# Kernel optimization log

Measured on AMD Instinct MI355X. Metric: run time of the kernel, lower is better.

## Reference

```python
import jax, jax.numpy as jnp
import numpy as np

N = 100000   # nodes
E = 600000   # edges
DIN = 128
H = 128
DOUT = 64
EPS = 1e-5   # BatchNorm1d default eps


def setup_inputs() -> dict:
    key = jax.random.key(0)
    ks = jax.random.split(key, 16)
    w = lambda k, shape: jax.random.normal(k, shape, jnp.float32) * 0.05
    return {
        "x": jax.random.normal(ks[0], (N, DIN), jnp.float32),
        "edge_index": jax.random.randint(ks[1], (2, E), 0, N),
        # layer 1: SAGEConv(DIN -> H)  (lin_l on aggregated neighbors w/ bias, lin_r on root)
        "Wl1": w(ks[2], (DIN, H)), "bl1": jnp.zeros((H,), jnp.float32), "Wr1": w(ks[3], (DIN, H)),
        "g1": jnp.ones((H,), jnp.float32), "be1": jnp.zeros((H,), jnp.float32),
        "rm1": jax.random.normal(ks[4], (H,), jnp.float32) * 0.1,
        "rv1": jax.random.uniform(ks[5], (H,), jnp.float32, 0.5, 1.5),
        # layer 2: SAGEConv(H -> H)
        "Wl2": w(ks[6], (H, H)), "bl2": jnp.zeros((H,), jnp.float32), "Wr2": w(ks[7], (H, H)),
        "g2": jnp.ones((H,), jnp.float32), "be2": jnp.zeros((H,), jnp.float32),
        "rm2": jax.random.normal(ks[8], (H,), jnp.float32) * 0.1,
        "rv2": jax.random.uniform(ks[9], (H,), jnp.float32, 0.5, 1.5),
        # layer 3: SAGEConv(H -> DOUT), no BN/ReLU after
        "Wl3": w(ks[10], (H, DOUT)), "bl3": jnp.zeros((DOUT,), jnp.float32), "Wr3": w(ks[11], (H, DOUT)),
    }


def _sage_conv(x, src, dst, Wl, bl, Wr):
    # mean-aggregate source features at targets, then lin_l(agg) + b + lin_r(x)
    agg = jax.ops.segment_sum(x[src], dst, num_segments=N)          # [N, d]
    deg = jax.ops.segment_sum(jnp.ones((src.shape[0],), x.dtype), dst, num_segments=N)
    agg = agg / jnp.maximum(deg, 1.0)[:, None]
    return agg @ Wl + bl + x @ Wr


def _bn_eval(h, g, b, rm, rv):
    return (h - rm) * (g * jax.lax.rsqrt(rv + EPS)) + b


def reference(x, edge_index, Wl1, bl1, Wr1, g1, be1, rm1, rv1,
              Wl2, bl2, Wr2, g2, be2, rm2, rv2, Wl3, bl3, Wr3):
    src, dst = edge_index[0], edge_index[1]
    h = jax.nn.relu(_bn_eval(_sage_conv(x, src, dst, Wl1, bl1, Wr1), g1, be1, rm1, rv1))
    h = jax.nn.relu(_bn_eval(_sage_conv(h, src, dst, Wl2, bl2, Wr2), g2, be2, rm2, rv2))
    return _sage_conv(h, src, dst, Wl3, bl3, Wr3)   # [N, DOUT]
```

## Files before the change

### kernel.cpp

```cpp
#include <hip/hip_runtime.h>

#define CAP 48

typedef short  s8v  __attribute__((ext_vector_type(8)));
typedef float  f4v  __attribute__((ext_vector_type(4)));

__device__ __forceinline__ unsigned short f2bf(float f) {
    unsigned u = __float_as_uint(f);
    u += 0x7FFFu + ((u >> 16) & 1u);
    return (unsigned short)(u >> 16);
}
__device__ __forceinline__ float bflo(unsigned v) { return __uint_as_float(v << 16); }
__device__ __forceinline__ float bfhi(unsigned v) { return __uint_as_float(v & 0xffff0000u); }

#define ACC8(A_, v) do { (A_)[0]+=bflo((v).x); (A_)[1]+=bfhi((v).x); (A_)[2]+=bflo((v).y); (A_)[3]+=bfhi((v).y); \
                         (A_)[4]+=bflo((v).z); (A_)[5]+=bfhi((v).z); (A_)[6]+=bflo((v).w); (A_)[7]+=bfhi((v).w); } while(0)

__global__ __launch_bounds__(256) void k_prep(const int* __restrict__ src, const int* __restrict__ dst, int E,
                                              int* __restrict__ cnt, int* __restrict__ bucket,
                                              const float* __restrict__ x, unsigned short* __restrict__ xb, int n4,
                                              const float* W0, const float* W1, const float* W2,
                                              const float* W3, const float* W4, const float* W5,
                                              unsigned short* P0, unsigned short* P1, unsigned short* P2,
                                              unsigned short* P3, unsigned short* P4, unsigned short* P5,
                                              const float* g1, const float* be1, const float* rm1, const float* rv1, const float* bl1,
                                              const float* g2, const float* be2, const float* rm2, const float* rv2, const float* bl2,
                                              float* P,
                                              unsigned short* hb, unsigned short* hb2, unsigned short* t3b, int N,
                                              int nbBucket, int nbCvt) {
    int b = blockIdx.x;
    const int tid = threadIdx.x;
    if (b < nbBucket) {
        int e = b * 256 + tid;
        if (e < E) {
            int d = dst[e];
            int slot = atomicAdd(&cnt[d], 1);
            if (slot < CAP) bucket[(size_t)d * CAP + slot] = src[e];
        }
        return;
    }
    b -= nbBucket;
    if (b < nbCvt) {
        int i = b * 256 + tid;
        if (i < n4) {
            float4 v = ((const float4*)x)[i];
            ushort4 o;
            o.x = f2bf(v.x); o.y = f2bf(v.y); o.z = f2bf(v.z); o.w = f2bf(v.w);
            ((ushort4*)xb)[i] = o;
        }
        return;
    }
    b -= nbCvt;
    const int px = b & 63;
    const int py = b >> 6;
    if (py == 6) {
        if (px == 0 && tid < 128) {
            int i = tid;
            float s1 = g1[i] * rsqrtf(rv1[i] + 1e-5f);
            P[i]       = s1;
            P[128 + i] = (bl1[i] - rm1[i]) * s1 + be1[i];
            float s2 = g2[i] * rsqrtf(rv2[i] + 1e-5f);
            P[256 + i] = s2;
            P[384 + i] = (bl2[i] - rm2[i]) * s2 + be2[i];
            xb [(size_t)N * 128 + i] = 0;
            hb [(size_t)N * 128 + i] = 0;
            hb2[(size_t)N * 128 + i] = 0;
            if (i < 64) t3b[(size_t)N * 64 + i] = 0;
        }
        return;
    }
    const float* W; unsigned short* Pk; int JD;
    switch (py) {
        case 0: W = W0; Pk = P0; JD = 128; break;
        case 1: W = W1; Pk = P1; JD = 128; break;
        case 2: W = W2; Pk = P2; JD = 128; break;
        case 3: W = W3; Pk = P3; JD = 128; break;
        case 4: W = W4; Pk = P4; JD = 64;  break;
        default:W = W5; Pk = P5; JD = 64;  break;
    }
    int o = px * 256 + tid;
    if (o >= 128 * JD) return;
    int j    = o & 7;
    int lane = (o >> 3) & 63;
    int t    = o >> 9;
    int nt   = t % (JD / 16);
    int kt   = t / (JD / 16);
    int k = kt * 32 + (lane >> 4) * 8 + j;
    int nn = nt * 16 + (lane & 15);
    Pk[o] = f2bf(W[(size_t)k * JD + nn]);
}

template<bool T3>
__global__ __launch_bounds__(256) void k_fused(const unsigned short* __restrict__ feat,
                                               const int* __restrict__ cnt, const int* __restrict__ bucket,
                                               const unsigned short* __restrict__ Bl, const unsigned short* __restrict__ Br,
                                               const float* __restrict__ scale, const float* __restrict__ shift,
                                               unsigned short* __restrict__ out,
                                               const unsigned short* __restrict__ W3p, unsigned short* __restrict__ t3,
                                               int n, int units) {
    __shared__ unsigned short sA[32 * 136];
    __shared__ unsigned short sH[T3 ? 32 * 136 : 8];
    const int tid  = threadIdx.x;
    const int wave = tid >> 6;
    const int lane = tid & 63;

    for (int u = blockIdx.x; u < units; u += gridDim.x) {
        const int nb0 = u * 32;

        {
            const int q4   = lane >> 4;
            const int li   = lane & 15;
            const int base = q4 << 4;
            const uint4* inp = (const uint4*)feat;
            int rows[2], cs[2], idxs[2];
            #pragma unroll
            for (int t = 0; t < 2; t++) {
                rows[t] = wave * 8 + t * 4 + q4;
                int node = nb0 + rows[t];
                bool ok = node < n;
                int c = ok ? cnt[node] : 0; if (c > CAP) c = CAP;
                cs[t] = c;
                idxs[t] = (ok && li < c) ? bucket[(size_t)node * CAP + li] : n;
            }
            #pragma unroll
            for (int t = 0; t < 2; t++) {
                const int c = cs[t];
                float a[8] = {0.f, 0.f, 0.f, 0.f, 0.f, 0.f, 0.f, 0.f};
                if (c > 0) {
                    #pragma unroll
                    for (int uu = 0; uu < 8; uu++) {
                        int idx = __shfl(idxs[t], base + uu);
                        uint4 v = inp[(size_t)idx * 16 + li];
                        ACC8(a, v);
                    }
                }
                if (c > 8) {
                    #pragma unroll
                    for (int uu = 8; uu < 16; uu++) {
                        int idx = __shfl(idxs[t], base + uu);
                        uint4 v = inp[(size_t)idx * 16 + li];
                        ACC8(a, v);
                    }
                }
                const int node = nb0 + rows[t];
                for (int s = 16; s < c; s++) {
                    int idx = bucket[(size_t)node * CAP + s];
                    uint4 v = inp[(size_t)idx * 16 + li];
                    ACC8(a, v);
                }
                if (node < n) {
                    float iv = 1.0f / fmaxf((float)c, 1.0f);
                    uint4 o;
                    o.x = (unsigned)f2bf(a[0] * iv) | ((unsigned)f2bf(a[1] * iv) << 16);
                    o.y = (unsigned)f2bf(a[2] * iv) | ((unsigned)f2bf(a[3] * iv) << 16);
                    o.z = (unsigned)f2bf(a[4] * iv) | ((unsigned)f2bf(a[5] * iv) << 16);
                    o.w = (unsigned)f2bf(a[6] * iv) | ((unsigned)f2bf(a[7] * iv) << 16);
                    *(uint4*)(sA + rows[t] * 136 + li * 8) = o;
                }
            }
        }
        __syncthreads();

        const int m = lane & 15;
        const int q = lane >> 4;
        const int nt0 = wave * 2;
        const int rg0 = min(nb0 + m,      n - 1);
        const int rg1 = min(nb0 + 16 + m, n - 1);

        f4v acc[2][2];
        #pragma unroll
        for (int mt = 0; mt < 2; mt++)
            #pragma unroll
            for (int c = 0; c < 2; c++) {
                acc[mt][c][0] = 0.f; acc[mt][c][1] = 0.f; acc[mt][c][2] = 0.f; acc[mt][c][3] = 0.f;
            }

        #pragma unroll
        for (int kt = 0; kt < 4; kt++) {
            const int ko = kt * 32 + q * 8;
            s8v a0 = *(const s8v*)(sA + m * 136 + ko);
            s8v a1 = *(const s8v*)(sA + (16 + m) * 136 + ko);
            s8v a0d = *(const s8v*)(feat + (size_t)rg0 * 128 + ko);
            s8v a1d = *(const s8v*)(feat + (size_t)rg1 * 128 + ko);
            #pragma unroll
            for (int c = 0; c < 2; c++) {
                s8v b  = *(const s8v*)(Bl + ((size_t)(kt * 8 + nt0 + c) * 64 + lane) * 8);
                acc[0][c] = __builtin_amdgcn_mfma_f32_16x16x32_bf16(a0, b, acc[0][c], 0, 0, 0);
                acc[1][c] = __builtin_amdgcn_mfma_f32_16x16x32_bf16(a1, b, acc[1][c], 0, 0, 0);
                s8v b2 = *(const s8v*)(Br + ((size_t)(kt * 8 + nt0 + c) * 64 + lane) * 8);
                acc[0][c] = __builtin_amdgcn_mfma_f32_16x16x32_bf16(a0d, b2, acc[0][c], 0, 0, 0);
                acc[1][c] = __builtin_amdgcn_mfma_f32_16x16x32_bf16(a1d, b2, acc[1][c], 0, 0, 0);
            }
        }

        float scv[2], shv[2];
        #pragma unroll
        for (int c = 0; c < 2; c++) {
            int col = (nt0 + c) * 16 + m;
            scv[c] = scale[col]; shv[c] = shift[col];
        }
        #pragma unroll
        for (int mt = 0; mt < 2; mt++) {
            #pragma unroll
            for (int reg = 0; reg < 4; reg++) {
                int rloc = mt * 16 + q * 4 + reg;
                int row  = nb0 + rloc;
                if (row < n) {
                    #pragma unroll
                    for (int c = 0; c < 2; c++) {
                        int col = (nt0 + c) * 16 + m;
                        float v = fmaxf(acc[mt][c][reg] * scv[c] + shv[c], 0.f);
                        unsigned short uq = f2bf(v);
                        out[(size_t)row * 128 + col] = uq;
                        if constexpr (T3) sH[rloc * 136 + col] = uq;
                    }
                }
            }
        }

        if constexpr (T3) {
            __syncthreads();
            f4v a3c[2];
            #pragma unroll
            for (int mt = 0; mt < 2; mt++) { a3c[mt][0] = 0.f; a3c[mt][1] = 0.f; a3c[mt][2] = 0.f; a3c[mt][3] = 0.f; }
            #pragma unroll
            for (int kt = 0; kt < 4; kt++) {
                const int ko = kt * 32 + q * 8;
                s8v a0 = *(const s8v*)(sH + m * 136 + ko);
                s8v a1 = *(const s8v*)(sH + (16 + m) * 136 + ko);
                s8v b  = *(const s8v*)(W3p + ((size_t)(kt * 4 + wave) * 64 + lane) * 8);
                a3c[0] = __builtin_amdgcn_mfma_f32_16x16x32_bf16(a0, b, a3c[0], 0, 0, 0);
                a3c[1] = __builtin_amdgcn_mfma_f32_16x16x32_bf16(a1, b, a3c[1], 0, 0, 0);
            }
            #pragma unroll
            for (int mt = 0; mt < 2; mt++) {
                #pragma unroll
                for (int reg = 0; reg < 4; reg++) {
                    int row = nb0 + mt * 16 + q * 4 + reg;
                    if (row < n) t3[(size_t)row * 64 + wave * 16 + m] = f2bf(a3c[mt][reg]);
                }
            }
        }
        __syncthreads();
    }
}

__global__ __launch_bounds__(256) void k_final(const unsigned short* __restrict__ hb2,
                                               const unsigned short* __restrict__ t3,
                                               const int* __restrict__ cnt, const int* __restrict__ bucket,
                                               const unsigned short* __restrict__ Bp, const float* __restrict__ bias,
                                               float* __restrict__ outf, int n, int units) {
    __shared__ float sG[32 * 68];
    const int tid  = threadIdx.x;
    const int wave = tid >> 6;
    const int lane = tid & 63;

    for (int u = blockIdx.x; u < units; u += gridDim.x) {
        const int nb0 = u * 32;

        {
            const int e8   = lane >> 3;
            const int li   = lane & 7;
            const int base = e8 << 3;
            const uint4* inp = (const uint4*)t3;
            const int row  = wave * 8 + e8;
            const int node = nb0 + row;
            const bool ok  = node < n;
            int c = ok ? cnt[node] : 0; if (c > CAP) c = CAP;
            int idx1 = (ok && li < c)     ? bucket[(size_t)node * CAP + li]     : n;
            int idx2 = (ok && li + 8 < c) ? bucket[(size_t)node * CAP + li + 8] : n;
            float a[8] = {0.f, 0.f, 0.f, 0.f, 0.f, 0.f, 0.f, 0.f};
            if (c > 0) {
                #pragma unroll
                for (int uu = 0; uu < 8; uu++) {
                    int idx = __shfl(idx1, base + uu);
                    uint4 v = inp[(size_t)idx * 8 + li];
                    ACC8(a, v);
                }
            }
            if (c > 8) {
                #pragma unroll
                for (int uu = 0; uu < 8; uu++) {
                    int idx = __shfl(idx2, base + uu);
                    uint4 v = inp[(size_t)idx * 8 + li];
                    ACC8(a, v);
                }
            }
            for (int s = 16; s < c; s++) {
                int idx = bucket[(size_t)node * CAP + s];
                uint4 v = inp[(size_t)idx * 8 + li];
                ACC8(a, v);
            }
            if (ok) {
                float iv = 1.0f / fmaxf((float)c, 1.0f);
                float4 o1; o1.x = a[0] * iv; o1.y = a[1] * iv; o1.z = a[2] * iv; o1.w = a[3] * iv;
                float4 o2; o2.x = a[4] * iv; o2.y = a[5] * iv; o2.z = a[6] * iv; o2.w = a[7] * iv;
                *(float4*)(sG + row * 68 + li * 8)     = o1;
                *(float4*)(sG + row * 68 + li * 8 + 4) = o2;
            }
        }
        __syncthreads();

        const int m = lane & 15;
        const int q = lane >> 4;
        const int rg0 = min(nb0 + m,      n - 1);
        const int rg1 = min(nb0 + 16 + m, n - 1);

        f4v acc[2];
        #pragma unroll
        for (int mt = 0; mt < 2; mt++) { acc[mt][0] = 0.f; acc[mt][1] = 0.f; acc[mt][2] = 0.f; acc[mt][3] = 0.f; }

        #pragma unroll
        for (int kt = 0; kt < 4; kt++) {
            const int ko = kt * 32 + q * 8;
            s8v a0 = *(const s8v*)(hb2 + (size_t)rg0 * 128 + ko);
            s8v a1 = *(const s8v*)(hb2 + (size_t)rg1 * 128 + ko);
            s8v b  = *(const s8v*)(Bp + ((size_t)(kt * 4 + wave) * 64 + lane) * 8);
            acc[0] = __builtin_amdgcn_mfma_f32_16x16x32_bf16(a0, b, acc[0], 0, 0, 0);
            acc[1] = __builtin_amdgcn_mfma_f32_16x16x32_bf16(a1, b, acc[1], 0, 0, 0);
        }

        const int col = wave * 16 + m;
        const float bv = bias[col];
        #pragma unroll
        for (int mt = 0; mt < 2; mt++) {
            #pragma unroll
            for (int reg = 0; reg < 4; reg++) {
                int rloc = mt * 16 + q * 4 + reg;
                int row  = nb0 + rloc;
                if (row < n) outf[(size_t)row * 64 + col] = acc[mt][reg] + sG[rloc * 68 + col] + bv;
            }
        }
        __syncthreads();
    }
}

extern "C" void kernel_launch(void* const* d_in, const int* in_sizes, int n_in,
                              void* d_out, int out_size, void* d_ws, size_t ws_size,
                              hipStream_t stream) {
    const float* x   = (const float*)d_in[0];
    const int*   ei  = (const int*)d_in[1];
    const float* Wl1 = (const float*)d_in[2];
    const float* bl1 = (const float*)d_in[3];
    const float* Wr1 = (const float*)d_in[4];
    const float* g1  = (const float*)d_in[5];
    const float* be1 = (const float*)d_in[6];
    const float* rm1 = (const float*)d_in[7];
    const float* rv1 = (const float*)d_in[8];
    const float* Wl2 = (const float*)d_in[9];
    const float* bl2 = (const float*)d_in[10];
    const float* Wr2 = (const float*)d_in[11];
    const float* g2  = (const float*)d_in[12];
    const float* be2 = (const float*)d_in[13];
    const float* rm2 = (const float*)d_in[14];
    const float* rv2 = (const float*)d_in[15];
    const float* Wl3 = (const float*)d_in[16];
    const float* bl3 = (const float*)d_in[17];
    const float* Wr3 = (const float*)d_in[18];

    const int N = in_sizes[0] / 128;
    const int E = in_sizes[1] / 2;
    const int* src = ei;
    const int* dst = ei + E;

    char* w = (char*)d_ws;
    auto au = [](size_t v) { return (v + 1023) & ~(size_t)1023; };
    size_t off = 0;
    int*            cnt    = (int*)(w + off);            off += au((size_t)N * 4);
    int*            bucket = (int*)(w + off);            off += au((size_t)N * CAP * 4);
    unsigned short* xb     = (unsigned short*)(w + off); off += au((size_t)(N + 1) * 128 * 2);
    unsigned short* hb     = (unsigned short*)(w + off); off += au((size_t)(N + 1) * 128 * 2);
    unsigned short* hb2    = (unsigned short*)(w + off); off += au((size_t)(N + 1) * 128 * 2);
    unsigned short* t3b    = (unsigned short*)(w + off); off += au((size_t)(N + 1) * 64 * 2);
    unsigned short* Wp[6];
    Wp[0] = (unsigned short*)(w + off); off += au(128 * 128 * 2);
    Wp[1] = (unsigned short*)(w + off); off += au(128 * 128 * 2);
    Wp[2] = (unsigned short*)(w + off); off += au(128 * 128 * 2);
    Wp[3] = (unsigned short*)(w + off); off += au(128 * 128 * 2);
    Wp[4] = (unsigned short*)(w + off); off += au(128 * 64 * 2);
    Wp[5] = (unsigned short*)(w + off); off += au(128 * 64 * 2);
    float* P = (float*)(w + off); off += 2048;
    (void)ws_size; (void)n_in;

    hipMemsetAsync(cnt, 0, (size_t)N * 4, stream);

    const int n4 = N * 32;
    const int nbBucket = (E + 255) / 256;
    const int nbCvt    = (n4 + 255) / 256;
    k_prep<<<nbBucket + nbCvt + 448, 256, 0, stream>>>(src, dst, E, cnt, bucket,
                                                       x, xb, n4,
                                                       Wl1, Wr1, Wl2, Wr2, Wl3, Wr3,
                                                       Wp[0], Wp[1], Wp[2], Wp[3], Wp[4], Wp[5],
                                                       g1, be1, rm1, rv1, bl1, g2, be2, rm2, rv2, bl2, P,
                                                       hb, hb2, t3b, N, nbBucket, nbCvt);

    const int units = (N + 31) / 32;
    const int grid  = (units + 1) / 2;

    k_fused<false><<<grid, 256, 0, stream>>>(xb, cnt, bucket, Wp[0], Wp[1],
                                             P, P + 128, hb, nullptr, nullptr, N, units);
    k_fused<true><<<grid, 256, 0, stream>>>(hb, cnt, bucket, Wp[2], Wp[3],
                                            P + 256, P + 384, hb2, Wp[4], t3b, N, units);
    k_final<<<grid, 256, 0, stream>>>(hb2, t3b, cnt, bucket, Wp[5], bl3, (float*)d_out, N, units);
}
```

Baseline: 305.3 us.

## Make each wave own 16 rows end to end and drop block barriers

The fused and final kernels now have each wave gather, aggregate and multiply its own 16 rows across all output columns, so no __syncthreads is needed between the gather and MFMA phases. The grid-stride loop is replaced by one 64-node block per launch index. The aim is to remove barrier stalls and let waves overlap gather latency with other waves' matrix work. In exchange each wave reloads every B tile itself, which adds L1/L2 traffic, and it holds more accumulator registers.

```diff
diff --git a/kernel.cpp b/kernel.cpp
--- a/kernel.cpp
+++ b/kernel.cpp
@@ -97,151 +97,130 @@
                                                const float* __restrict__ scale, const float* __restrict__ shift,
                                                unsigned short* __restrict__ out,
                                                const unsigned short* __restrict__ W3p, unsigned short* __restrict__ t3,
-                                               int n, int units) {
-    __shared__ unsigned short sA[32 * 136];
-    __shared__ unsigned short sH[T3 ? 32 * 136 : 8];
+                                               int n) {
+    __shared__ unsigned short sA[64 * 136];
     const int tid  = threadIdx.x;
     const int wave = tid >> 6;
     const int lane = tid & 63;
-
-    for (int u = blockIdx.x; u < units; u += gridDim.x) {
-        const int nb0 = u * 32;
-
-        {
-            const int q4   = lane >> 4;
-            const int li   = lane & 15;
-            const int base = q4 << 4;
-            const uint4* inp = (const uint4*)feat;
-            int rows[2], cs[2], idxs[2];
-            #pragma unroll
-            for (int t = 0; t < 2; t++) {
-                rows[t] = wave * 8 + t * 4 + q4;
-                int node = nb0 + rows[t];
-                bool ok = node < n;
-                int c = ok ? cnt[node] : 0; if (c > CAP) c = CAP;
-                cs[t] = c;
-                idxs[t] = (ok && li < c) ? bucket[(size_t)node * CAP + li] : n;
-            }
-            #pragma unroll
-            for (int t = 0; t < 2; t++) {
-                const int c = cs[t];
-                float a[8] = {0.f, 0.f, 0.f, 0.f, 0.f, 0.f, 0.f, 0.f};
-                if (c > 0) {
-                    #pragma unroll
-                    for (int uu = 0; uu < 8; uu++) {
-                        int idx = __shfl(idxs[t], base + uu);
-                        uint4 v = inp[(size_t)idx * 16 + li];
-                        ACC8(a, v);
-                    }
-                }
-                if (c > 8) {
-                    #pragma unroll
-                    for (int uu = 8; uu < 16; uu++) {
-                        int idx = __shfl(idxs[t], base + uu);
-                        uint4 v = inp[(size_t)idx * 16 + li];
-                        ACC8(a, v);
-                    }
-                }
-                const int node = nb0 + rows[t];
-                for (int s = 16; s < c; s++) {
-                    int idx = bucket[(size_t)node * CAP + s];
+    const int nb0  = blockIdx.x * 64;
+    const int wb   = nb0 + wave * 16;
+    if (wb >= n) return;
+
+    {
+        const int q4   = lane >> 4;
+        const int li   = lane & 15;
+        const int base = q4 << 4;
+        const uint4* inp = (const uint4*)feat;
+        int cs[4], idxs[4];
+        #pragma unroll
+        for (int t = 0; t < 4; t++) {
+            int node = wb + t * 4 + q4;
+            bool ok = node < n;
+            int c = ok ? cnt[node] : 0; if (c > CAP) c = CAP;
+            cs[t] = c;
+            idxs[t] = (ok && li < c) ? bucket[(size_t)node * CAP + li] : n;
+        }
+        #pragma unroll
+        for (int t = 0; t < 4; t++) {
+            const int c = cs[t];
+            float a[8] = {0.f, 0.f, 0.f, 0.f, 0.f, 0.f, 0.f, 0.f};
+            if (c > 0) {
+                #pragma unroll
+                for (int uu = 0; uu < 8; uu++) {
+                    int idx = __shfl(idxs[t], base + uu);
                     uint4 v = inp[(size_t)idx * 16 + li];
                     ACC8(a, v);
                 }
-                if (node < n) {
-                    float iv = 1.0f / fmaxf((float)c, 1.0f);
-                    uint4 o;
-                    o.x = (unsigned)f2bf(a[0] * iv) | ((unsigned)f2bf(a[1] * iv) << 16);
-                    o.y = (unsigned)f2bf(a[2] * iv) | ((unsigned)f2bf(a[3] * iv) << 16);
-                    o.z = (unsigned)f2bf(a[4] * iv) | ((unsigned)f2bf(a[5] * iv) << 16);
-                    o.w = (unsigned)f2bf(a[6] * iv) | ((unsigned)f2bf(a[7] * iv) << 16);
-                    *(uint4*)(sA + rows[t] * 136 + li * 8) = o;
+            }
+            if (c > 8) {
+                #pragma unroll
+                for (int uu = 8; uu < 16; uu++) {
+                    int idx = __shfl(idxs[t], base + uu);
+                    uint4 v = inp[(size_t)idx * 16 + li];
+                    ACC8(a, v);
                 }
             }
-        }
-        __syncthreads();
-
-        const int m = lane & 15;
-        const int q = lane >> 4;
-        const int nt0 = wave * 2;
-        const int rg0 = min(nb0 + m,      n - 1);
-        const int rg1 = min(nb0 + 16 + m, n - 1);
-
-        f4v acc[2][2];
-        #pragma unroll
-        for (int mt = 0; mt < 2; mt++)
-            #pragma unroll
-            for (int c = 0; c < 2; c++) {
-                acc[mt][c][0] = 0.f; acc[mt][c][1] = 0.f; acc[mt][c][2] = 0.f; acc[mt][c][3] = 0.f;
-            }
-
+            const int node = wb + t * 4 + q4;
+            for (int s = 16; s < c; s++) {
+                int idx = bucket[(size_t)node * CAP + s];
+                uint4 v = inp[(size_t)idx * 16 + li];
+                ACC8(a, v);
+            }
+            if (node < n) {
+                float iv = 1.0f / fmaxf((float)c, 1.0f);
+                uint4 o;
+                o.x = (unsigned)f2bf(a[0] * iv) | ((unsigned)f2bf(a[1] * iv) << 16);
+                o.y = (unsigned)f2bf(a[2] * iv) | ((unsigned)f2bf(a[3] * iv) << 16);
+                o.z = (unsigned)f2bf(a[4] * iv) | ((unsigned)f2bf(a[5] * iv) << 16);
+                o.w = (unsigned)f2bf(a[6] * iv) | ((unsigned)f2bf(a[7] * iv) << 16);
+                *(uint4*)(sA + (wave * 16 + t * 4 + q4) * 136 + li * 8) = o;
+            }
+        }
+    }
+
+    const int m = lane & 15;
+    const int q = lane >> 4;
+    const int arow = wave * 16 + m;
+    const int rg = min(wb + m, n - 1);
+
+    f4v acc[8];
+    #pragma unroll
+    for (int nt = 0; nt < 8; nt++) { acc[nt][0] = 0.f; acc[nt][1] = 0.f; acc[nt][2] = 0.f; acc[nt][3] = 0.f; }
+
+    #pragma unroll
+    for (int kt = 0; kt < 4; kt++) {
+        const int ko = kt * 32 + q * 8;
+        s8v a0  = *(const s8v*)(sA + arow * 136 + ko);
+        s8v a0d = *(const s8v*)(feat + (size_t)rg * 128 + ko);
+        #pragma unroll
+        for (int nt = 0; nt < 8; nt++) {
+            s8v b  = *(const s8v*)(Bl + ((size_t)(kt * 8 + nt) * 64 + lane) * 8);
+            acc[nt] = __builtin_amdgcn_mfma_f32_16x16x32_bf16(a0, b, acc[nt], 0, 0, 0);
+            s8v b2 = *(const s8v*)(Br + ((size_t)(kt * 8 + nt) * 64 + lane) * 8);
+            acc[nt] = __builtin_amdgcn_mfma_f32_16x16x32_bf16(a0d, b2, acc[nt], 0, 0, 0);
+        }
+    }
+
+    #pragma unroll
+    for (int nt = 0; nt < 8; nt++) {
+        const int col = nt * 16 + m;
+        const float sc = scale[col];
+        const float sh = shift[col];
+        #pragma unroll
+        for (int reg = 0; reg < 4; reg++) {
+            int rloc = wave * 16 + q * 4 + reg;
+            int row  = nb0 + rloc;
+            if (row < n) {
+                float v = fmaxf(acc[nt][reg] * sc + sh, 0.f);
+                unsigned short uq = f2bf(v);
+                out[(size_t)row * 128 + col] = uq;
+                if constexpr (T3) sA[rloc * 136 + col] = uq;
+            }
+        }
+    }
+
+    if constexpr (T3) {
+        f4v a3c[4];
+        #pragma unroll
+        for (int nt = 0; nt < 4; nt++) { a3c[nt][0] = 0.f; a3c[nt][1] = 0.f; a3c[nt][2] = 0.f; a3c[nt][3] = 0.f; }
         #pragma unroll
         for (int kt = 0; kt < 4; kt++) {
             const int ko = kt * 32 + q * 8;
-            s8v a0 = *(const s8v*)(sA + m * 136 + ko);
-            s8v a1 = *(const s8v*)(sA + (16 + m) * 136 + ko);
-            s8v a0d = *(const s8v*)(feat + (size_t)rg0 * 128 + ko);
-            s8v a1d = *(const s8v*)(feat + (size_t)rg1 * 128 + ko);
+            s8v a0 = *(const s8v*)(sA + arow * 136 + ko);
             #pragma unroll
-            for (int c = 0; c < 2; c++) {
-                s8v b  = *(const s8v*)(Bl + ((size_t)(kt * 8 + nt0 + c) * 64 + lane) * 8);
-                acc[0][c] = __builtin_amdgcn_mfma_f32_16x16x32_bf16(a0, b, acc[0][c], 0, 0, 0);
-                acc[1][c] = __builtin_amdgcn_mfma_f32_16x16x32_bf16(a1, b, acc[1][c], 0, 0, 0);
-                s8v b2 = *(const s8v*)(Br + ((size_t)(kt * 8 + nt0 + c) * 64 + lane) * 8);
-                acc[0][c] = __builtin_amdgcn_mfma_f32_16x16x32_bf16(a0d, b2, acc[0][c], 0, 0, 0);
-                acc[1][c] = __builtin_amdgcn_mfma_f32_16x16x32_bf16(a1d, b2, acc[1][c], 0, 0, 0);
-            }
-        }
-
-        float scv[2], shv[2];
-        #pragma unroll
-        for (int c = 0; c < 2; c++) {
-            int col = (nt0 + c) * 16 + m;
-            scv[c] = scale[col]; shv[c] = shift[col];
-        }
-        #pragma unroll
-        for (int mt = 0; mt < 2; mt++) {
+            for (int nt = 0; nt < 4; nt++) {
+                s8v b = *(const s8v*)(W3p + ((size_t)(kt * 4 + nt) * 64 + lane) * 8);
+                a3c[nt] = __builtin_amdgcn_mfma_f32_16x16x32_bf16(a0, b, a3c[nt], 0, 0, 0);
+            }
+        }
+        #pragma unroll
+        for (int nt = 0; nt < 4; nt++) {
             #pragma unroll
             for (int reg = 0; reg < 4; reg++) {
-                int rloc = mt * 16 + q * 4 + reg;
-                int row  = nb0 + rloc;
-                if (row < n) {
-                    #pragma unroll
-                    for (int c = 0; c < 2; c++) {
-                        int col = (nt0 + c) * 16 + m;
-                        float v = fmaxf(acc[mt][c][reg] * scv[c] + shv[c], 0.f);
-                        unsigned short uq = f2bf(v);
-                        out[(size_t)row * 128 + col] = uq;
-                        if constexpr (T3) sH[rloc * 136 + col] = uq;
-                    }
-                }
-            }
-        }
-
-        if constexpr (T3) {
-            __syncthreads();
-            f4v a3c[2];
-            #pragma unroll
-            for (int mt = 0; mt < 2; mt++) { a3c[mt][0] = 0.f; a3c[mt][1] = 0.f; a3c[mt][2] = 0.f; a3c[mt][3] = 0.f; }
-            #pragma unroll
-            for (int kt = 0; kt < 4; kt++) {
-                const int ko = kt * 32 + q * 8;
-                s8v a0 = *(const s8v*)(sH + m * 136 + ko);
-                s8v a1 = *(const s8v*)(sH + (16 + m) * 136 + ko);
-                s8v b  = *(const s8v*)(W3p + ((size_t)(kt * 4 + wave) * 64 + lane) * 8);
-                a3c[0] = __builtin_amdgcn_mfma_f32_16x16x32_bf16(a0, b, a3c[0], 0, 0, 0);
-                a3c[1] = __builtin_amdgcn_mfma_f32_16x16x32_bf16(a1, b, a3c[1], 0, 0, 0);
-            }
-            #pragma unroll
-            for (int mt = 0; mt < 2; mt++) {
-                #pragma unroll
-                for (int reg = 0; reg < 4; reg++) {
-                    int row = nb0 + mt * 16 + q * 4 + reg;
-                    if (row < n) t3[(size_t)row * 64 + wave * 16 + m] = f2bf(a3c[mt][reg]);
-                }
-            }
-        }
-        __syncthreads();
+                int row = nb0 + wave * 16 + q * 4 + reg;
+                if (row < n) t3[(size_t)row * 64 + nt * 16 + m] = f2bf(a3c[nt][reg]);
+            }
+        }
     }
 }
 
@@ -249,22 +228,24 @@
                                                const unsigned short* __restrict__ t3,
                                                const int* __restrict__ cnt, const int* __restrict__ bucket,
                                                const unsigned short* __restrict__ Bp, const float* __restrict__ bias,
-                                               float* __restrict__ outf, int n, int units) {
-    __shared__ float sG[32 * 68];
+                                               float* __restrict__ outf, int n) {
+    __shared__ float sG[64 * 68];
     const int tid  = threadIdx.x;
     const int wave = tid >> 6;
     const int lane = tid & 63;
-
-    for (int u = blockIdx.x; u < units; u += gridDim.x) {
-        const int nb0 = u * 32;
-
-        {
-            const int e8   = lane >> 3;
-            const int li   = lane & 7;
-            const int base = e8 << 3;
-            const uint4* inp = (const uint4*)t3;
-            const int row  = wave * 8 + e8;
-            const int node = nb0 + row;
+    const int nb0  = blockIdx.x * 64;
+    const int wb   = nb0 + wave * 16;
+    if (wb >= n) return;
+
+    {
+        const int e8   = lane >> 3;
+        const int li   = lane & 7;
+        const int base = e8 << 3;
+        const uint4* inp = (const uint4*)t3;
+        #pragma unroll
+        for (int t = 0; t < 2; t++) {
+            const int trow = t * 8 + e8;
+            const int node = wb + trow;
             const bool ok  = node < n;
             int c = ok ? cnt[node] : 0; if (c > CAP) c = CAP;
             int idx1 = (ok && li < c)     ? bucket[(size_t)node * CAP + li]     : n;
@@ -295,43 +276,41 @@
                 float iv = 1.0f / fmaxf((float)c, 1.0f);
                 float4 o1; o1.x = a[0] * iv; o1.y = a[1] * iv; o1.z = a[2] * iv; o1.w = a[3] * iv;
                 float4 o2; o2.x = a[4] * iv; o2.y = a[5] * iv; o2.z = a[6] * iv; o2.w = a[7] * iv;
-                *(float4*)(sG + row * 68 + li * 8)     = o1;
-                *(float4*)(sG + row * 68 + li * 8 + 4) = o2;
-            }
-        }
-        __syncthreads();
-
-        const int m = lane & 15;
-        const int q = lane >> 4;
-        const int rg0 = min(nb0 + m,      n - 1);
-        const int rg1 = min(nb0 + 16 + m, n - 1);
-
-        f4v acc[2];
-        #pragma unroll
-        for (int mt = 0; mt < 2; mt++) { acc[mt][0] = 0.f; acc[mt][1] = 0.f; acc[mt][2] = 0.f; acc[mt][3] = 0.f; }
-
-        #pragma unroll
-        for (int kt = 0; kt < 4; kt++) {
-            const int ko = kt * 32 + q * 8;
-            s8v a0 = *(const s8v*)(hb2 + (size_t)rg0 * 128 + ko);
-            s8v a1 = *(const s8v*)(hb2 + (size_t)rg1 * 128 + ko);
-            s8v b  = *(const s8v*)(Bp + ((size_t)(kt * 4 + wave) * 64 + lane) * 8);
-            acc[0] = __builtin_amdgcn_mfma_f32_16x16x32_bf16(a0, b, acc[0], 0, 0, 0);
-            acc[1] = __builtin_amdgcn_mfma_f32_16x16x32_bf16(a1, b, acc[1], 0, 0, 0);
-        }
-
-        const int col = wave * 16 + m;
+                *(float4*)(sG + (wave * 16 + trow) * 68 + li * 8)     = o1;
+                *(float4*)(sG + (wave * 16 + trow) * 68 + li * 8 + 4) = o2;
+            }
+        }
+    }
+
+    const int m = lane & 15;
+    const int q = lane >> 4;
+    const int rg = min(wb + m, n - 1);
+
+    f4v acc[4];
+    #pragma unroll
+    for (int nt = 0; nt < 4; nt++) { acc[nt][0] = 0.f; acc[nt][1] = 0.f; acc[nt][2] = 0.f; acc[nt][3] = 0.f; }
+
+    #pragma unroll
+    for (int kt = 0; kt < 4; kt++) {
+        const int ko = kt * 32 + q * 8;
+        s8v a0 = *(const s8v*)(hb2 + (size_t)rg * 128 + ko);
+        #pragma unroll
+        for (int nt = 0; nt < 4; nt++) {
+            s8v b = *(const s8v*)(Bp + ((size_t)(kt * 4 + nt) * 64 + lane) * 8);
+            acc[nt] = __builtin_amdgcn_mfma_f32_16x16x32_bf16(a0, b, acc[nt], 0, 0, 0);
+        }
+    }
+
+    #pragma unroll
+    for (int nt = 0; nt < 4; nt++) {
+        const int col = nt * 16 + m;
         const float bv = bias[col];
         #pragma unroll
-        for (int mt = 0; mt < 2; mt++) {
-            #pragma unroll
-            for (int reg = 0; reg < 4; reg++) {
-                int rloc = mt * 16 + q * 4 + reg;
-                int row  = nb0 + rloc;
-                if (row < n) outf[(size_t)row * 64 + col] = acc[mt][reg] + sG[rloc * 68 + col] + bv;
-            }
-        }
-        __syncthreads();
+        for (int reg = 0; reg < 4; reg++) {
+            int rloc = wave * 16 + q * 4 + reg;
+            int row  = nb0 + rloc;
+            if (row < n) outf[(size_t)row * 64 + col] = acc[nt][reg] + sG[rloc * 68 + col] + bv;
+        }
     }
 }
 
@@ -394,12 +373,11 @@
                                                        g1, be1, rm1, rv1, bl1, g2, be2, rm2, rv2, bl2, P,
                                                        hb, hb2, t3b, N, nbBucket, nbCvt);
 
-    const int units = (N + 31) / 32;
-    const int grid  = (units + 1) / 2;
+    const int grid = (N + 63) / 64;
 
     k_fused<false><<<grid, 256, 0, stream>>>(xb, cnt, bucket, Wp[0], Wp[1],
-                                             P, P + 128, hb, nullptr, nullptr, N, units);
+                                             P, P + 128, hb, nullptr, nullptr, N);
     k_fused<true><<<grid, 256, 0, stream>>>(hb, cnt, bucket, Wp[2], Wp[3],
-                                            P + 256, P + 384, hb2, Wp[4], t3b, N, units);
-    k_final<<<grid, 256, 0, stream>>>(hb2, t3b, cnt, bucket, Wp[5], bl3, (float*)d_out, N, units);
-}
+                                            P + 256, P + 384, hb2, Wp[4], t3b, N);
+    k_final<<<grid, 256, 0, stream>>>(hb2, t3b, cnt, bucket, Wp[5], bl3, (float*)d_out, N);
+}
```

New measurement: 299.7 us. About the same (-1.8%).
